# Performance work log

Hardware: AMD Instinct MI355X
Metric: run time of the kernel (lower is better)

## Reference

```python
import jax, jax.numpy as jnp
import numpy as np

B, T, P, D = 32, 8, 196, 768
M = 10
NUM_CLASSES = 100
NUM_IDX = 98
P_MASK = 0.5


def setup_inputs() -> dict:
    key = jax.random.key(0)
    ks = jax.random.split(key, 16)
    s = 0.02
    inp = {
        'visual': jax.random.normal(ks[0], (B, T * P, D), jnp.float32),
        'audio': jax.random.normal(ks[1], (B, D), jnp.float32),
        'causal': jax.random.normal(ks[2], (B, M, D), jnp.float32),
        'random_mask': jax.random.uniform(ks[3], (B, T, P, D)) < P_MASK,
        'Wa': jax.random.normal(ks[4], (D, D), jnp.float32) * s,
        'ba': jnp.zeros((D,), jnp.float32),
        'Wv': jax.random.normal(ks[5], (D, D), jnp.float32) * s,
        'bv': jnp.zeros((D,), jnp.float32),
        'Waa': jax.random.normal(ks[6], (D, D), jnp.float32) * s,
        'baa': jnp.zeros((D,), jnp.float32),
        'Wav': jax.random.normal(ks[7], (D, D), jnp.float32) * s,
        'bav': jnp.zeros((D,), jnp.float32),
        'Wf': jax.random.normal(ks[8], (D, D), jnp.float32) * s,
        'bf': jnp.zeros((D,), jnp.float32),
        'Wf2': jax.random.normal(ks[9], (D, 1), jnp.float32) * s,
        'bf2': jnp.zeros((1,), jnp.float32),
        'Wc': jax.random.normal(ks[10], (D, NUM_CLASSES), jnp.float32) * s,
        'bc': jnp.zeros((NUM_CLASSES,), jnp.float32),
        'causal_param': jnp.zeros((1,), jnp.float32),
    }
    return inp


def reference(visual, audio, causal, random_mask, Wa, ba, Wv, bv, Waa, baa,
              Wav, bav, Wf, bf, Wf2, bf2, Wc, bc, causal_param):
    vis = visual.reshape(visual.shape[0], T, -1, D)  # [B,8,196,768]

    # causal_intervention_mean_feature4
    cp = jax.nn.sigmoid(causal_param)                 # soft_clamp2, [1]
    feats = causal @ Wf + bf                          # [B,M,D]
    feats2 = jnp.swapaxes(causal @ Wf2 + bf2, 1, 2)   # [B,1,M]
    fw = jax.nn.softmax(jnp.tanh(feats), axis=1)      # [B,M,D]
    ci = jnp.einsum('bom,bmd->bd', feats2, fw * causal)  # bmm + squeeze
    audio2 = cp * ci + audio                          # [B,D]

    # audio_visual_attention1
    pa = jnp.tanh(audio2 @ Waa + baa)                 # [B,D]
    pv = jnp.tanh(vis @ Wav + bav)                    # [B,T,P,D]
    sscore = pv * pa[:, None, None, :]                # einsum ijkd,id->ijkd
    sattn = jax.nn.softmax(sscore, axis=2)            # softmax over patches
    patch = jnp.sum(sattn, axis=-1)                   # [B,T,P]
    thresh = jnp.sort(patch, axis=-1)[:, :, NUM_IDX]  # per (b,t) threshold
    spa_mask = patch < thresh[:, :, None]             # [B,T,P]
    final_mask = ~(spa_mask[..., None] & random_mask) # [B,T,P,D]
    sfilt = jnp.where(final_mask, sattn, 0.0)

    sav = jnp.sum(sfilt * pv, axis=2)                 # [B,T,D]
    tattn = jax.nn.softmax(sav * pa[:, None, :], axis=1)

    vp = jnp.sum(sfilt * vis, axis=2)                 # [B,T,D]
    vp = jnp.sum(tattn * vp, axis=1)                  # [B,D]

    af = jax.nn.relu(audio2 @ Wa + ba)
    vf = jax.nn.relu(vp @ Wv + bv)
    logits = (af + vf) @ Wc + bc                      # [B,num_classes]
    return logits
```

## Files before the change

### kernel.cpp

```cpp
#include <hip/hip_runtime.h>
#include <hip/hip_bf16.h>
#include <hip/hip_fp16.h>
#include <math.h>

#define BB 32
#define TT 8
#define PP 196
#define DD 768
#define MM 10
#define NCLS 100
#define NIDX 98

typedef __attribute__((ext_vector_type(8))) short short8v;
typedef __attribute__((ext_vector_type(4))) float float4v;

__device__ __forceinline__ float fast_tanh(float x) {
    float e = __expf(2.0f * x);
    return 1.0f - 2.0f / (e + 1.0f);
}
__device__ __forceinline__ unsigned short f2bf(float x) {
    __hip_bfloat16 h = __float2bfloat16(x);
    return *(unsigned short*)&h;
}
__device__ __forceinline__ float bf2f(unsigned short h) {
    return __uint_as_float(((unsigned)h) << 16);
}
__device__ __forceinline__ unsigned short f2h(float x) {
    __half h = __float2half(x);
    return *(unsigned short*)&h;
}
__device__ __forceinline__ float h2f(unsigned short u) {
    __half h = *(__half*)&u;
    return __half2float(h);
}

__global__ __launch_bounds__(768) void k_prep_all(
    const float* __restrict__ vis, unsigned short* __restrict__ visb,
    const unsigned int* __restrict__ rm, int* __restrict__ mode,
    const float* __restrict__ Wav, unsigned short* __restrict__ Wht,
    const float* __restrict__ causal, const float* __restrict__ Wf,
    const float* __restrict__ Wf2,
    float* __restrict__ pf, float* __restrict__ pf2) {
    int t = threadIdx.x;
    int bid = blockIdx.x;
    if (bid < 1024) {
        const size_t NC = (size_t)BB * TT * PP * DD / 8;
        size_t gid = (size_t)bid * 768 + t;
        for (size_t i = gid; i < NC; i += 1024 * 768) {
            const float4* s = (const float4*)(vis + i * 8);
            float4 x = s[0], y = s[1];
            __hip_bfloat162 h;
            unsigned int u0, u1, u2, u3;
            h = __float22bfloat162_rn(make_float2(x.x, x.y)); u0 = *(unsigned int*)&h;
            h = __float22bfloat162_rn(make_float2(x.z, x.w)); u1 = *(unsigned int*)&h;
            h = __float22bfloat162_rn(make_float2(y.x, y.y)); u2 = *(unsigned int*)&h;
            h = __float22bfloat162_rn(make_float2(y.z, y.w)); u3 = *(unsigned int*)&h;
            uint4 o; o.x = u0; o.y = u1; o.z = u2; o.w = u3;
            ((uint4*)visb)[i] = o;
        }
        if (bid == 0) {
            __shared__ int f_ni, f_nf;
            if (t == 0) { f_ni = 0; f_nf = 0; }
            __syncthreads();
            int ni = 0, nf = 0;
            for (int i = t; i < 16384; i += 768) {
                unsigned int v = rm[i];
                ni |= (v > 1u) ? 1 : 0;
                nf |= (v != 0u && v != 0x3F800000u) ? 1 : 0;
            }
            if (ni) atomicOr(&f_ni, 1);
            if (nf) atomicOr(&f_nf, 1);
            __syncthreads();
            if (t == 0) *mode = f_ni ? (f_nf ? 2 : 1) : 0;
        }
    } else if (bid < 1600) {
        __shared__ float tile[32][33];
        int bb = bid - 1024;
        int bn = (bb % 24) * 32;
        int bk = (bb / 24) * 32;
        if (t < 256) {
            int tx = t & 31, ty = t >> 5;
            #pragma unroll
            for (int i = 0; i < 4; ++i)
                tile[ty + i * 8][tx] = Wav[(size_t)(bk + ty + i * 8) * DD + bn + tx];
        }
        __syncthreads();
        if (t < 256) {
            int tx = t & 31, ty = t >> 5;
            #pragma unroll
            for (int i = 0; i < 4; ++i) {
                int n = bn + ty + i * 8, k = bk + tx;
                Wht[(size_t)n * DD + k] = f2bf(tile[tx][ty + i * 8]);
            }
        }
    } else {
        __shared__ float cs[MM][256];
        __shared__ float red[MM][12];
        int bb = bid - 1600;
        int b = bb % 32, kc = bb / 32;
        int k0 = kc * 256;
        for (int i = t; i < MM * 256; i += 768)
            cs[i >> 8][i & 255] = causal[((size_t)b * MM + (i >> 8)) * DD + k0 + (i & 255)];
        __syncthreads();
        int wave = t >> 6, lane = t & 63;
        float w2v = (t < 256) ? Wf2[k0 + t] : 0.f;
        #pragma unroll
        for (int m = 0; m < MM; ++m) {
            float p = (t < 256) ? cs[m][t] * w2v : 0.f;
            #pragma unroll
            for (int o = 32; o > 0; o >>= 1) p += __shfl_down(p, o);
            if (lane == 0) red[m][wave] = p;
        }
        __syncthreads();
        if (t < MM) {
            float s = 0.f;
            #pragma unroll
            for (int wv = 0; wv < 4; ++wv) s += red[t][wv];
            pf2[(b * 3 + kc) * MM + t] = s;
        }
        float acc[MM];
        #pragma unroll
        for (int m = 0; m < MM; ++m) acc[m] = 0.f;
        #pragma unroll 4
        for (int k = 0; k < 256; ++k) {
            float wv = Wf[(size_t)(k0 + k) * DD + t];
            #pragma unroll
            for (int m = 0; m < MM; ++m) acc[m] = fmaf(cs[m][k], wv, acc[m]);
        }
        #pragma unroll
        for (int m = 0; m < MM; ++m)
            pf[(((size_t)b * 3 + kc) * MM + m) * DD + t] = acc[m];
    }
}

__global__ __launch_bounds__(768) void k_audio2a(
    const float* __restrict__ causal, const float* __restrict__ audio,
    const float* __restrict__ pf, const float* __restrict__ pf2,
    const float* __restrict__ bf, const float* __restrict__ bf2,
    const float* __restrict__ cparam, float* __restrict__ a2) {
    int b = blockIdx.x;
    int t = threadIdx.x;
    float cp = 1.0f / (1.0f + __expf(-cparam[0]));
    float tf[MM], f2[MM];
    float mx = -1e30f;
    #pragma unroll
    for (int m = 0; m < MM; ++m) {
        float acc = bf[t];
        float s2 = bf2[0];
        #pragma unroll
        for (int kc = 0; kc < 3; ++kc) {
            acc += pf[(((size_t)b * 3 + kc) * MM + m) * DD + t];
            s2 += pf2[(b * 3 + kc) * MM + m];
        }
        tf[m] = fast_tanh(acc);
        f2[m] = s2;
        mx = fmaxf(mx, tf[m]);
    }
    float s = 0.f;
    #pragma unroll
    for (int m = 0; m < MM; ++m) { tf[m] = __expf(tf[m] - mx); s += tf[m]; }
    float inv = 1.0f / s;
    float ci = 0.f;
    #pragma unroll
    for (int m = 0; m < MM; ++m)
        ci += f2[m] * (tf[m] * inv) * causal[((size_t)b * MM + m) * DD + t];
    a2[(size_t)b * DD + t] = cp * ci + audio[(size_t)b * DD + t];
}

__global__ __launch_bounds__(256) void k_audio2b(
    const float* __restrict__ a2,
    const float* __restrict__ Waa, const float* __restrict__ baa,
    const float* __restrict__ Wa, const float* __restrict__ ba,
    float* __restrict__ pa, float* __restrict__ af, float* __restrict__ colsum) {
    int gid0 = (blockIdx.y * 24 + blockIdx.x) * 256 + threadIdx.x;
    for (int i = gid0; i < BB * TT * DD; i += 48 * 256) colsum[i] = 0.f;
    __shared__ float a2s[16][DD + 4];
    int sel = blockIdx.y;
    const float* W = sel ? Wa : Waa;
    int t = threadIdx.x;
    int c = blockIdx.x * 32 + (t & 31);
    int slot = t >> 5;
    float bias = sel ? ba[c] : baa[c];
    #pragma unroll
    for (int g = 0; g < 2; ++g) {
        if (g) __syncthreads();
        for (int i = t; i < 16 * DD; i += 256)
            a2s[i / DD][i % DD] = a2[(size_t)(g * 16 + i / DD) * DD + i % DD];
        __syncthreads();
        float acc0 = 0.f, acc1 = 0.f;
        #pragma unroll 8
        for (int k = 0; k < DD; ++k) {
            float wv = W[(size_t)k * DD + c];
            acc0 = fmaf(a2s[slot][k], wv, acc0);
            acc1 = fmaf(a2s[slot + 8][k], wv, acc1);
        }
        int b0 = g * 16 + slot, b1 = b0 + 8;
        if (sel == 0) {
            pa[(size_t)b0 * DD + c] = fast_tanh(acc0 + bias);
            pa[(size_t)b1 * DD + c] = fast_tanh(acc1 + bias);
        } else {
            af[(size_t)b0 * DD + c] = fmaxf(acc0 + bias, 0.f);
            af[(size_t)b1 * DD + c] = fmaxf(acc1 + bias, 0.f);
        }
    }
}

__global__ __launch_bounds__(256, 2) void k_pv_mfma(
    const unsigned short* __restrict__ visb, const unsigned short* __restrict__ Wht,
    const float* __restrict__ bav, const float* __restrict__ pa,
    unsigned short* __restrict__ pvh, float* __restrict__ colsum)
{
    __shared__ unsigned short As[2][128 * 64];
    __shared__ unsigned short Bs[2][128 * 64];
    int wg = blockIdx.x;
    int lin = (wg & 7) * 294 + (wg >> 3);
    int mt = lin / 6, nt = lin % 6;
    int i0 = mt * 128, n0 = nt * 128;
    int t = threadIdx.x, w = t >> 6, l = t & 63;
    int wm = (w >> 1) * 64, wn = (w & 1) * 64;

    float4v zero4 = {0.f, 0.f, 0.f, 0.f};
    float4v acc[4][4];
    #pragma unroll
    for (int a = 0; a < 4; ++a)
        #pragma unroll
        for (int b = 0; b < 4; ++b) acc[a][b] = zero4;

    int brow[4], bcs[4];
    #pragma unroll
    for (int j = 0; j < 4; ++j) {
        int row = (w * 4 + j) * 8 + (l >> 3);
        brow[j] = row;
        bcs[j] = (l & 7) ^ (row & 7);
    }

#define STAGE(bb, wnd_)                                                          \
    {                                                                            \
        int kw_ = (wnd_) * 64;                                                   \
        _Pragma("unroll")                                                        \
        for (int j = 0; j < 4; ++j) {                                            \
            size_t aoff_ = (size_t)(i0 + brow[j]) * DD + kw_ + bcs[j] * 8;       \
            __builtin_amdgcn_global_load_lds(                                    \
                (const __attribute__((address_space(1))) unsigned int*)(visb + aoff_), \
                (__attribute__((address_space(3))) unsigned int*)&As[bb][(w * 4 + j) * 512], \
                16, 0, 0);                                                       \
            size_t boff_ = (size_t)(n0 + brow[j]) * DD + kw_ + bcs[j] * 8;       \
            __builtin_amdgcn_global_load_lds(                                    \
                (const __attribute__((address_space(1))) unsigned int*)(Wht + boff_), \
                (__attribute__((address_space(3))) unsigned int*)&Bs[bb][(w * 4 + j) * 512], \
                16, 0, 0);                                                       \
        }                                                                        \
    }

    STAGE(0, 0);
    for (int wnd = 0; wnd < 12; ++wnd) {
        int cur = wnd & 1;
        if (wnd < 11) {
            STAGE(cur ^ 1, wnd + 1);
            asm volatile("s_waitcnt vmcnt(8)" ::: "memory");
        } else {
            asm volatile("s_waitcnt vmcnt(0)" ::: "memory");
        }
        __builtin_amdgcn_s_barrier();
        __builtin_amdgcn_s_setprio(1);
        #pragma unroll
        for (int kk = 0; kk < 2; ++kk) {
            short8v ahf[4], bhf[4];
            #pragma unroll
            for (int mr = 0; mr < 4; ++mr) {
                int row = wm + mr * 16 + (l & 15);
                int c = kk * 4 + (l >> 4);
                ahf[mr] = *(const short8v*)&As[cur][row * 64 + ((c ^ (row & 7)) * 8)];
            }
            #pragma unroll
            for (int nc = 0; nc < 4; ++nc) {
                int row = wn + nc * 16 + (l & 15);
                int c = kk * 4 + (l >> 4);
                bhf[nc] = *(const short8v*)&Bs[cur][row * 64 + ((c ^ (row & 7)) * 8)];
            }
            #pragma unroll
            for (int mr = 0; mr < 4; ++mr)
                #pragma unroll
                for (int nc = 0; nc < 4; ++nc)
                    acc[mr][nc] = __builtin_amdgcn_mfma_f32_16x16x32_bf16(
                        ahf[mr], bhf[nc], acc[mr][nc], 0, 0, 0);
        }
        __builtin_amdgcn_s_setprio(0);
        asm volatile("s_waitcnt lgkmcnt(0)" ::: "memory");
        __builtin_amdgcn_sched_barrier(0);
        __builtin_amdgcn_s_barrier();
    }
#undef STAGE
    unsigned short* Cl = &As[0][0];
    float* cred = (float*)&Bs[0][0];
    if (t < 256) cred[t] = 0.f;
    __syncthreads();
    int bt0 = i0 / PP;
    int btbound = (bt0 + 1) * PP;
    #pragma unroll
    for (int nc = 0; nc < 4; ++nc) {
        int cl = wn + nc * 16 + (l & 15);
        int col = n0 + cl;
        float bias = bav[col];
        #pragma unroll
        for (int mr = 0; mr < 4; ++mr) {
            int lr0 = wm + mr * 16 + ((l >> 4) << 2);
            int row0 = i0 + lr0;
            int bq = row0 / (TT * PP);
            float pav = pa[(size_t)bq * DD + col];
            float esum = 0.f;
            #pragma unroll
            for (int v = 0; v < 4; ++v) {
                unsigned short pb = f2h(fast_tanh(acc[mr][nc][v] + bias));
                int lr = lr0 + v;
                int boff = lr * 256 + ((cl * 2) ^ ((lr & 7) << 4));
                *(unsigned short*)((char*)Cl + boff) = pb;
                esum += __expf(h2f(pb) * pav);
            }
            int btg = (row0 >= btbound) ? 1 : 0;
            atomicAdd(&cred[btg * 128 + cl], esum);
        }
    }
    __syncthreads();
    #pragma unroll
    for (int rb = 0; rb < 2; ++rb) {
        int lr = (t >> 2) + rb * 64;
        size_t grow = (size_t)(i0 + lr) * DD + n0;
        #pragma unroll
        for (int q = 0; q < 4; ++q) {
            int ch = (t & 3) + q * 4;
            int boff = lr * 256 + ((ch * 16) ^ ((lr & 7) << 4));
            uint4 val = *(uint4*)((char*)Cl + boff);
            *(uint4*)(pvh + grow + ch * 8) = val;
        }
    }
    if (t < 256) {
        int btg = t >> 7, cl = t & 127;
        if (btg == 0 || btbound < i0 + 128)
            atomicAdd(&colsum[(size_t)(bt0 + btg) * DD + n0 + cl], cred[t]);
    }
}

__global__ __launch_bounds__(768) void k_patch(
    const unsigned short* __restrict__ pvh, const float* __restrict__ pa,
    const float* __restrict__ colsum, unsigned char* __restrict__ spa_g) {
    int bt = blockIdx.x;
    int b = bt >> 3;
    size_t base = (size_t)bt * PP * DD;
    __shared__ float2 pi[DD];
    __shared__ float patch[PP];
    int t = threadIdx.x;
    float pav = pa[(size_t)b * DD + t];
    float inv = 1.0f / colsum[(size_t)bt * DD + t];
    pi[t] = make_float2(pav, inv);
    __syncthreads();
    int wave = t >> 6, lane = t & 63;
    for (int p = wave; p < PP; p += 12) {
        const uint2* rv = (const uint2*)(pvh + base + (size_t)p * DD);
        float sum = 0.f;
        #pragma unroll
        for (int j = lane; j < 192; j += 64) {
            uint2 v = rv[j];
            int c = j * 4;
            float2 q0 = pi[c], q1 = pi[c + 1], q2 = pi[c + 2], q3 = pi[c + 3];
            sum += __expf(h2f((unsigned short)(v.x & 0xFFFFu)) * q0.x) * q0.y
                 + __expf(h2f((unsigned short)(v.x >> 16)) * q1.x) * q1.y
                 + __expf(h2f((unsigned short)(v.y & 0xFFFFu)) * q2.x) * q2.y
                 + __expf(h2f((unsigned short)(v.y >> 16)) * q3.x) * q3.y;
        }
        #pragma unroll
        for (int o = 32; o > 0; o >>= 1) sum += __shfl_down(sum, o);
        if (lane == 0) patch[p] = sum;
    }
    __syncthreads();
    if (t < PP) {
        float x = patch[t];
        int c = 0;
        for (int q = 0; q < PP; ++q) c += (patch[q] <= x) ? 1 : 0;
        spa_g[bt * PP + t] = (c <= NIDX) ? 1 : 0;
    }
}

__global__ __launch_bounds__(768) void k_masked(
    const unsigned short* __restrict__ pvh, const unsigned short* __restrict__ visb,
    const void* __restrict__ rmask, const int* __restrict__ mode_p,
    const float* __restrict__ pa, const float* __restrict__ colsum,
    const unsigned char* __restrict__ spa_g,
    float* __restrict__ sav, float* __restrict__ vpt) {
    int bt = blockIdx.x;
    int qd = blockIdx.y;
    int b = bt >> 3;
    size_t base = (size_t)bt * PP * DD;
    __shared__ unsigned char spa[PP];
    __shared__ float red_s[4][192];
    __shared__ float red_v[4][192];
    int t = threadIdx.x;
    if (t < PP) spa[t] = spa_g[bt * PP + t];
    int pg = t / 192;
    int c = t - pg * 192;
    int col = qd * 192 + c;
    int p0 = pg * 49, p1 = p0 + 49;
    float pav = pa[(size_t)b * DD + col];
    float inv = 1.0f / colsum[(size_t)bt * DD + col];
    __syncthreads();
    const unsigned short* pvb = pvh + base + col;
    const unsigned short* vib = visb + base + col;
    float sava = 0.f, vpa = 0.f;
    int mode = *mode_p;
    if (mode == 0) {
        const int* mb = (const int*)rmask + base + col;
        #pragma unroll 7
        for (int p = p0; p < p1; ++p) {
            float pvv = h2f(pvb[(size_t)p * DD]);
            float sa = __expf(pvv * pav) * inv;
            bool km = !(spa[p] && (mb[(size_t)p * DD] != 0));
            if (km) { sava = fmaf(sa, pvv, sava); vpa = fmaf(sa, bf2f(vib[(size_t)p * DD]), vpa); }
        }
    } else if (mode == 1) {
        const float* mb = (const float*)rmask + base + col;
        #pragma unroll 7
        for (int p = p0; p < p1; ++p) {
            float pvv = h2f(pvb[(size_t)p * DD]);
            float sa = __expf(pvv * pav) * inv;
            bool km = !(spa[p] && (mb[(size_t)p * DD] != 0.f));
            if (km) { sava = fmaf(sa, pvv, sava); vpa = fmaf(sa, bf2f(vib[(size_t)p * DD]), vpa); }
        }
    } else {
        const unsigned char* mb = (const unsigned char*)rmask + base + col;
        #pragma unroll 7
        for (int p = p0; p < p1; ++p) {
            float pvv = h2f(pvb[(size_t)p * DD]);
            float sa = __expf(pvv * pav) * inv;
            bool km = !(spa[p] && (mb[(size_t)p * DD] != 0));
            if (km) { sava = fmaf(sa, pvv, sava); vpa = fmaf(sa, bf2f(vib[(size_t)p * DD]), vpa); }
        }
    }
    red_s[pg][c] = sava;
    red_v[pg][c] = vpa;
    __syncthreads();
    if (t < 192) {
        int col2 = qd * 192 + t;
        sav[(size_t)bt * DD + col2] = red_s[0][t] + red_s[1][t] + red_s[2][t] + red_s[3][t];
        vpt[(size_t)bt * DD + col2] = red_v[0][t] + red_v[1][t] + red_v[2][t] + red_v[3][t];
    }
}

__global__ __launch_bounds__(768) void k_tail_a(
    const float* __restrict__ sav, const float* __restrict__ vpt,
    const float* __restrict__ pa, float* __restrict__ vp) {
    int b = blockIdx.x;
    int t = threadIdx.x;
    float pav = pa[(size_t)b * DD + t];
    float x[TT];
    float mx = -1e30f;
    #pragma unroll
    for (int k = 0; k < TT; ++k) {
        x[k] = sav[((size_t)b * TT + k) * DD + t] * pav;
        mx = fmaxf(mx, x[k]);
    }
    float s = 0.f;
    #pragma unroll
    for (int k = 0; k < TT; ++k) { x[k] = __expf(x[k] - mx); s += x[k]; }
    float inv = 1.0f / s;
    float acc = 0.f;
    #pragma unroll
    for (int k = 0; k < TT; ++k)
        acc += x[k] * inv * vpt[((size_t)b * TT + k) * DD + t];
    vp[(size_t)b * DD + t] = acc;
}

__global__ __launch_bounds__(256) void k_tail_b(
    const float* __restrict__ vp, const float* __restrict__ af,
    const float* __restrict__ Wv, const float* __restrict__ bv,
    float* __restrict__ h) {
    __shared__ float vs[16][DD + 4];
    int t = threadIdx.x;
    int c = blockIdx.x * 32 + (t & 31);
    int slot = t >> 5;
    float bias = bv[c];
    #pragma unroll
    for (int g = 0; g < 2; ++g) {
        if (g) __syncthreads();
        for (int i = t; i < 16 * DD; i += 256)
            vs[i / DD][i % DD] = vp[(size_t)(g * 16 + i / DD) * DD + i % DD];
        __syncthreads();
        float acc0 = 0.f, acc1 = 0.f;
        #pragma unroll 8
        for (int k = 0; k < DD; ++k) {
            float wv = Wv[(size_t)k * DD + c];
            acc0 = fmaf(vs[slot][k], wv, acc0);
            acc1 = fmaf(vs[slot + 8][k], wv, acc1);
        }
        int b0 = g * 16 + slot, b1 = b0 + 8;
        h[(size_t)b0 * DD + c] = fmaxf(acc0 + bias, 0.f) + af[(size_t)b0 * DD + c];
        h[(size_t)b1 * DD + c] = fmaxf(acc1 + bias, 0.f) + af[(size_t)b1 * DD + c];
    }
}

__global__ __launch_bounds__(256) void k_tail_c(
    const float* __restrict__ h, const float* __restrict__ Wc,
    const float* __restrict__ bc, float* __restrict__ out) {
    int t = threadIdx.x;
    int c = blockIdx.x * 8 + (t & 7);
    int b = t >> 3;
    if (c >= NCLS) return;
    float acc = bc[c];
    #pragma unroll 8
    for (int k = 0; k < DD; ++k)
        acc = fmaf(h[(size_t)b * DD + k], Wc[(size_t)k * NCLS + c], acc);
    out[(size_t)b * NCLS + c] = acc;
}

extern "C" void kernel_launch(void* const* d_in, const int* in_sizes, int n_in,
                              void* d_out, int out_size, void* d_ws, size_t ws_size,
                              hipStream_t stream) {
    const float* visual = (const float*)d_in[0];
    const float* audio  = (const float*)d_in[1];
    const float* causal = (const float*)d_in[2];
    const void*  rmask  = d_in[3];
    const float* Wa   = (const float*)d_in[4];
    const float* ba   = (const float*)d_in[5];
    const float* Wv   = (const float*)d_in[6];
    const float* bv   = (const float*)d_in[7];
    const float* Waa  = (const float*)d_in[8];
    const float* baa  = (const float*)d_in[9];
    const float* Wav  = (const float*)d_in[10];
    const float* bav  = (const float*)d_in[11];
    const float* Wf   = (const float*)d_in[12];
    const float* bf   = (const float*)d_in[13];
    const float* Wf2  = (const float*)d_in[14];
    const float* bf2  = (const float*)d_in[15];
    const float* Wc   = (const float*)d_in[16];
    const float* bc   = (const float*)d_in[17];
    const float* cpar = (const float*)d_in[18];
    float* out = (float*)d_out;

    const size_t NE = (size_t)BB * TT * PP * DD;
    unsigned short* Wht = (unsigned short*)d_ws;
    float* pfreg = (float*)(Wht + (size_t)DD * DD);
    float* colsum = pfreg;
    float* savw  = colsum + (size_t)BB * TT * DD;
    float* vptw  = savw + (size_t)BB * TT * DD;
    float* vpw   = vptw + (size_t)BB * TT * DD;
    float* hw    = vpw + (size_t)BB * DD;
    unsigned char* spa_g = (unsigned char*)(hw + (size_t)BB * DD);
    float* pf    = pfreg;
    float* pf2   = pfreg + (size_t)BB * 3 * MM * DD;
    float* a2w   = pf2 + 1024;
    float* paw   = a2w + (size_t)BB * DD;
    float* afw   = paw + (size_t)BB * DD;
    int*   modew = (int*)(afw + (size_t)BB * DD);
    unsigned short* visb = (unsigned short*)(modew + 16);
    unsigned short* pvh  = visb + NE;

    k_prep_all<<<1696, 768, 0, stream>>>(visual, visb, (const unsigned int*)rmask,
                                         modew, Wav, Wht, causal, Wf, Wf2, pf, pf2);
    k_audio2a<<<BB, 768, 0, stream>>>(causal, audio, pf, pf2, bf, bf2, cpar, a2w);
    k_audio2b<<<dim3(24, 2), 256, 0, stream>>>(a2w, Waa, baa, Wa, ba, paw, afw, colsum);
    k_pv_mfma<<<2352, 256, 0, stream>>>(visb, Wht, bav, paw, pvh, colsum);
    k_patch<<<BB * TT, 768, 0, stream>>>(pvh, paw, colsum, spa_g);
    k_masked<<<dim3(BB * TT, 4), 768, 0, stream>>>(pvh, visb, rmask, modew, paw,
                                                   colsum, spa_g, savw, vptw);
    k_tail_a<<<BB, 768, 0, stream>>>(savw, vptw, paw, vpw);
    k_tail_b<<<24, 256, 0, stream>>>(vpw, afw, Wv, bv, hw);
    k_tail_c<<<13, 256, 0, stream>>>(hw, Wc, bc, out);
}
```

Baseline: 506.4 us.

## Halve GEMM K-tile for higher occupancy and split patch reduction across column quarters

The MFMA GEMM now stages 32-wide K windows instead of 64, halving LDS usage and raising launch bounds to four waves per SIMD so more workgroups can be resident. The patch-score kernel is split over four column quarters writing partial sums, and the rank/threshold computation moves into the masked kernel, which sums the partials. This trades more barrier iterations and possible register pressure for better latency hiding and more parallelism in the patch stage.

```diff
diff --git a/kernel.cpp b/kernel.cpp
--- a/kernel.cpp
+++ b/kernel.cpp
@@ -205,13 +205,13 @@
     }
 }
 
-__global__ __launch_bounds__(256, 2) void k_pv_mfma(
+__global__ __launch_bounds__(256, 4) void k_pv_mfma(
     const unsigned short* __restrict__ visb, const unsigned short* __restrict__ Wht,
     const float* __restrict__ bav, const float* __restrict__ pa,
     unsigned short* __restrict__ pvh, float* __restrict__ colsum)
 {
-    __shared__ unsigned short As[2][128 * 64];
-    __shared__ unsigned short Bs[2][128 * 64];
+    __shared__ unsigned short SH[4][4096];
+    __shared__ float cred[256];
     int wg = blockIdx.x;
     int lin = (wg & 7) * 294 + (wg >> 3);
     int mt = lin / 6, nt = lin % 6;
@@ -226,57 +226,55 @@
         #pragma unroll
         for (int b = 0; b < 4; ++b) acc[a][b] = zero4;
 
-    int brow[4], bcs[4];
-    #pragma unroll
-    for (int j = 0; j < 4; ++j) {
-        int row = (w * 4 + j) * 8 + (l >> 3);
-        brow[j] = row;
-        bcs[j] = (l & 7) ^ (row & 7);
+    int srow[2], scs[2];
+    #pragma unroll
+    for (int j = 0; j < 2; ++j) {
+        int row = (w * 2 + j) * 16 + (l >> 2);
+        srow[j] = row;
+        scs[j] = (l & 3) ^ (row & 3);
     }
 
 #define STAGE(bb, wnd_)                                                          \
     {                                                                            \
-        int kw_ = (wnd_) * 64;                                                   \
+        int kw_ = (wnd_) * 32;                                                   \
         _Pragma("unroll")                                                        \
-        for (int j = 0; j < 4; ++j) {                                            \
-            size_t aoff_ = (size_t)(i0 + brow[j]) * DD + kw_ + bcs[j] * 8;       \
+        for (int j = 0; j < 2; ++j) {                                            \
+            size_t aoff_ = (size_t)(i0 + srow[j]) * DD + kw_ + scs[j] * 8;       \
             __builtin_amdgcn_global_load_lds(                                    \
                 (const __attribute__((address_space(1))) unsigned int*)(visb + aoff_), \
-                (__attribute__((address_space(3))) unsigned int*)&As[bb][(w * 4 + j) * 512], \
+                (__attribute__((address_space(3))) unsigned int*)&SH[bb][(w * 2 + j) * 512], \
                 16, 0, 0);                                                       \
-            size_t boff_ = (size_t)(n0 + brow[j]) * DD + kw_ + bcs[j] * 8;       \
+            size_t boff_ = (size_t)(n0 + srow[j]) * DD + kw_ + scs[j] * 8;       \
             __builtin_amdgcn_global_load_lds(                                    \
                 (const __attribute__((address_space(1))) unsigned int*)(Wht + boff_), \
-                (__attribute__((address_space(3))) unsigned int*)&Bs[bb][(w * 4 + j) * 512], \
+                (__attribute__((address_space(3))) unsigned int*)&SH[2 + bb][(w * 2 + j) * 512], \
                 16, 0, 0);                                                       \
         }                                                                        \
     }
 
     STAGE(0, 0);
-    for (int wnd = 0; wnd < 12; ++wnd) {
+    for (int wnd = 0; wnd < 24; ++wnd) {
         int cur = wnd & 1;
-        if (wnd < 11) {
+        if (wnd < 23) {
             STAGE(cur ^ 1, wnd + 1);
-            asm volatile("s_waitcnt vmcnt(8)" ::: "memory");
+            asm volatile("s_waitcnt vmcnt(4)" ::: "memory");
         } else {
             asm volatile("s_waitcnt vmcnt(0)" ::: "memory");
         }
         __builtin_amdgcn_s_barrier();
         __builtin_amdgcn_s_setprio(1);
-        #pragma unroll
-        for (int kk = 0; kk < 2; ++kk) {
+        {
             short8v ahf[4], bhf[4];
+            int cA = l >> 4;
             #pragma unroll
             for (int mr = 0; mr < 4; ++mr) {
                 int row = wm + mr * 16 + (l & 15);
-                int c = kk * 4 + (l >> 4);
-                ahf[mr] = *(const short8v*)&As[cur][row * 64 + ((c ^ (row & 7)) * 8)];
+                ahf[mr] = *(const short8v*)&SH[cur][row * 32 + ((cA ^ (row & 3)) * 8)];
             }
             #pragma unroll
             for (int nc = 0; nc < 4; ++nc) {
                 int row = wn + nc * 16 + (l & 15);
-                int c = kk * 4 + (l >> 4);
-                bhf[nc] = *(const short8v*)&Bs[cur][row * 64 + ((c ^ (row & 7)) * 8)];
+                bhf[nc] = *(const short8v*)&SH[2 + cur][row * 32 + ((cA ^ (row & 3)) * 8)];
             }
             #pragma unroll
             for (int mr = 0; mr < 4; ++mr)
@@ -291,8 +289,7 @@
         __builtin_amdgcn_s_barrier();
     }
 #undef STAGE
-    unsigned short* Cl = &As[0][0];
-    float* cred = (float*)&Bs[0][0];
+    unsigned short* Cl = &SH[0][0];
     if (t < 256) cred[t] = 0.f;
     __syncthreads();
     int bt0 = i0 / PP;
@@ -341,61 +338,66 @@
     }
 }
 
-__global__ __launch_bounds__(768) void k_patch(
+__global__ __launch_bounds__(768) void k_patchsum(
     const unsigned short* __restrict__ pvh, const float* __restrict__ pa,
-    const float* __restrict__ colsum, unsigned char* __restrict__ spa_g) {
-    int bt = blockIdx.x;
+    const float* __restrict__ colsum, float* __restrict__ patch_q) {
+    int bt = blockIdx.x, qd = blockIdx.y;
     int b = bt >> 3;
     size_t base = (size_t)bt * PP * DD;
-    __shared__ float2 pi[DD];
+    int c0 = qd * 192;
+    __shared__ float2 pi[192];
+    int t = threadIdx.x;
+    if (t < 192) {
+        int col = c0 + t;
+        pi[t] = make_float2(pa[(size_t)b * DD + col],
+                            1.0f / colsum[(size_t)bt * DD + col]);
+    }
+    __syncthreads();
+    int wv = t >> 6, l = t & 63;
+    for (int p = wv; p < PP; p += 12) {
+        float sum = 0.f;
+        if (l < 48) {
+            const uint2* rv = (const uint2*)(pvh + base + (size_t)p * DD + c0);
+            uint2 v = rv[l];
+            int c = l * 4;
+            float2 q0 = pi[c], q1 = pi[c + 1], q2 = pi[c + 2], q3 = pi[c + 3];
+            sum = __expf(h2f((unsigned short)(v.x & 0xFFFFu)) * q0.x) * q0.y
+                + __expf(h2f((unsigned short)(v.x >> 16)) * q1.x) * q1.y
+                + __expf(h2f((unsigned short)(v.y & 0xFFFFu)) * q2.x) * q2.y
+                + __expf(h2f((unsigned short)(v.y >> 16)) * q3.x) * q3.y;
+        }
+        #pragma unroll
+        for (int o = 32; o > 0; o >>= 1) sum += __shfl_down(sum, o);
+        if (l == 0) patch_q[((size_t)bt * PP + p) * 4 + qd] = sum;
+    }
+}
+
+__global__ __launch_bounds__(768) void k_masked(
+    const unsigned short* __restrict__ pvh, const unsigned short* __restrict__ visb,
+    const void* __restrict__ rmask, const int* __restrict__ mode_p,
+    const float* __restrict__ pa, const float* __restrict__ colsum,
+    const float* __restrict__ patch_q,
+    float* __restrict__ sav, float* __restrict__ vpt) {
+    int bt = blockIdx.x;
+    int qd = blockIdx.y;
+    int b = bt >> 3;
+    size_t base = (size_t)bt * PP * DD;
     __shared__ float patch[PP];
-    int t = threadIdx.x;
-    float pav = pa[(size_t)b * DD + t];
-    float inv = 1.0f / colsum[(size_t)bt * DD + t];
-    pi[t] = make_float2(pav, inv);
-    __syncthreads();
-    int wave = t >> 6, lane = t & 63;
-    for (int p = wave; p < PP; p += 12) {
-        const uint2* rv = (const uint2*)(pvh + base + (size_t)p * DD);
-        float sum = 0.f;
-        #pragma unroll
-        for (int j = lane; j < 192; j += 64) {
-            uint2 v = rv[j];
-            int c = j * 4;
-            float2 q0 = pi[c], q1 = pi[c + 1], q2 = pi[c + 2], q3 = pi[c + 3];
-            sum += __expf(h2f((unsigned short)(v.x & 0xFFFFu)) * q0.x) * q0.y
-                 + __expf(h2f((unsigned short)(v.x >> 16)) * q1.x) * q1.y
-                 + __expf(h2f((unsigned short)(v.y & 0xFFFFu)) * q2.x) * q2.y
-                 + __expf(h2f((unsigned short)(v.y >> 16)) * q3.x) * q3.y;
-        }
-        #pragma unroll
-        for (int o = 32; o > 0; o >>= 1) sum += __shfl_down(sum, o);
-        if (lane == 0) patch[p] = sum;
+    __shared__ unsigned char spa[PP];
+    __shared__ float red_s[4][192];
+    __shared__ float red_v[4][192];
+    int t = threadIdx.x;
+    if (t < PP) {
+        float4 v = *(const float4*)&patch_q[((size_t)bt * PP + t) * 4];
+        patch[t] = ((v.x + v.y) + v.z) + v.w;
     }
     __syncthreads();
     if (t < PP) {
         float x = patch[t];
         int c = 0;
         for (int q = 0; q < PP; ++q) c += (patch[q] <= x) ? 1 : 0;
-        spa_g[bt * PP + t] = (c <= NIDX) ? 1 : 0;
-    }
-}
-
-__global__ __launch_bounds__(768) void k_masked(
-    const unsigned short* __restrict__ pvh, const unsigned short* __restrict__ visb,
-    const void* __restrict__ rmask, const int* __restrict__ mode_p,
-    const float* __restrict__ pa, const float* __restrict__ colsum,
-    const unsigned char* __restrict__ spa_g,
-    float* __restrict__ sav, float* __restrict__ vpt) {
-    int bt = blockIdx.x;
-    int qd = blockIdx.y;
-    int b = bt >> 3;
-    size_t base = (size_t)bt * PP * DD;
-    __shared__ unsigned char spa[PP];
-    __shared__ float red_s[4][192];
-    __shared__ float red_v[4][192];
-    int t = threadIdx.x;
-    if (t < PP) spa[t] = spa_g[bt * PP + t];
+        spa[t] = (c <= NIDX) ? 1 : 0;
+    }
     int pg = t / 192;
     int c = t - pg * 192;
     int col = qd * 192 + c;
@@ -543,7 +545,6 @@
     float* vptw  = savw + (size_t)BB * TT * DD;
     float* vpw   = vptw + (size_t)BB * TT * DD;
     float* hw    = vpw + (size_t)BB * DD;
-    unsigned char* spa_g = (unsigned char*)(hw + (size_t)BB * DD);
     float* pf    = pfreg;
     float* pf2   = pfreg + (size_t)BB * 3 * MM * DD;
     float* a2w   = pf2 + 1024;
@@ -552,15 +553,16 @@
     int*   modew = (int*)(afw + (size_t)BB * DD);
     unsigned short* visb = (unsigned short*)(modew + 16);
     unsigned short* pvh  = visb + NE;
+    float* patchq = (float*)(pvh + NE);
 
     k_prep_all<<<1696, 768, 0, stream>>>(visual, visb, (const unsigned int*)rmask,
                                          modew, Wav, Wht, causal, Wf, Wf2, pf, pf2);
     k_audio2a<<<BB, 768, 0, stream>>>(causal, audio, pf, pf2, bf, bf2, cpar, a2w);
     k_audio2b<<<dim3(24, 2), 256, 0, stream>>>(a2w, Waa, baa, Wa, ba, paw, afw, colsum);
     k_pv_mfma<<<2352, 256, 0, stream>>>(visb, Wht, bav, paw, pvh, colsum);
-    k_patch<<<BB * TT, 768, 0, stream>>>(pvh, paw, colsum, spa_g);
+    k_patchsum<<<dim3(BB * TT, 4), 768, 0, stream>>>(pvh, paw, colsum, patchq);
     k_masked<<<dim3(BB * TT, 4), 768, 0, stream>>>(pvh, visb, rmask, modew, paw,
-                                                   colsum, spa_g, savw, vptw);
+                                                   colsum, patchq, savw, vptw);
     k_tail_a<<<BB, 768, 0, stream>>>(savw, vptw, paw, vpw);
     k_tail_b<<<24, 256, 0, stream>>>(vpw, afw, Wv, bv, hw);
     k_tail_c<<<13, 256, 0, stream>>>(hw, Wc, bc, out);
```

New measurement: 509.7 us. About the same (+0.6%).
